# Kernel tuning notes

Measured on AMD Instinct MI355X. Metric: run time of the kernel, lower is better.

The kernel has to match this reference:

```python
import jax, jax.numpy as jnp
import numpy as np

B, CIN, COUT, K = 16, 64, 64, 3
H = W = 192
DEG, HID = 64, 256


def setup_inputs() -> dict:
    key = jax.random.key(0)
    ks = jax.random.split(key, 6)
    x = jax.random.normal(ks[0], (B, CIN, H, W), dtype=jnp.float32)
    degradation_features = jax.random.normal(ks[1], (B, DEG), dtype=jnp.float32)
    # weight_generator: Linear(DEG,256) -> ReLU -> Linear(256, CIN*COUT*K*K)
    W1 = jax.random.normal(ks[2], (DEG, HID), dtype=jnp.float32) * (1.0 / np.sqrt(DEG))
    b1 = jax.random.normal(ks[3], (HID,), dtype=jnp.float32) * 0.01
    W2 = jax.random.normal(ks[4], (HID, CIN * COUT * K * K), dtype=jnp.float32) * (1.0 / np.sqrt(HID))
    b2 = jax.random.normal(ks[5], (CIN * COUT * K * K,), dtype=jnp.float32) * 0.01
    return {"x": x, "degradation_features": degradation_features,
            "W1": W1, "b1": b1, "W2": W2, "b2": b2}


def _forward(x, degradation_features, W1, b1, W2, b2):
    # generate per-sample conv weights: [B, COUT, CIN, K, K] (OIHW)
    h = jax.nn.relu(degradation_features @ W1 + b1)
    weights = (h @ W2 + b2).reshape(B, COUT, CIN, K, K)

    # Per-sample conv2d, NO padding (original loop omits padding arg -> VALID).
    def conv_one(xi, wi):
        # xi: [CIN, H, W], wi: [COUT, CIN, K, K]
        out = jax.lax.conv_general_dilated(
            xi[None], wi, window_strides=(1, 1), padding='VALID',
            dimension_numbers=('NCHW', 'OIHW', 'NCHW'))
        return out[0]  # [COUT, H-K+1, W-K+1]

    return jax.vmap(conv_one)(x, weights)


def reference(x, degradation_features, W1, b1, W2, b2):
    return _forward(x, degradation_features, W1, b1, W2, b2)
```

## Files before the change

kernel.cpp:

```cpp
#include <hip/hip_runtime.h>


typedef __bf16 bf16x8 __attribute__((ext_vector_type(8)));
typedef float  f32x4  __attribute__((ext_vector_type(4)));

#define NB   16
#define CIN  64
#define COUT 64
#define HW   192
#define OHW  190
#define NPIX (HW*HW)
#define NW2  (COUT*CIN*9)

__device__ __forceinline__ unsigned short f2bf(float f) {
    union { float f; unsigned int u; } v; v.f = f;
    unsigned int r = v.u + 0x7FFFu + ((v.u >> 16) & 1u);
    return (unsigned short)(r >> 16);
}
__device__ __forceinline__ float bf2f(unsigned short s) {
    union { unsigned int u; float f; } v; v.u = ((unsigned int)s) << 16;
    return v.f;
}

__device__ __forceinline__ void async_copy16(const void* gsrc, void* ldst) {
    __builtin_amdgcn_global_load_lds(
        (const __attribute__((address_space(1))) unsigned int*)gsrc,
        (__attribute__((address_space(3))) unsigned int*)ldst, 16, 0, 0);
}

__global__ void k1_hidden(const float* __restrict__ deg, const float* __restrict__ W1,
                          const float* __restrict__ b1, float* __restrict__ h) {
    int b = blockIdx.x, j = threadIdx.x;
    float acc = b1[j];
    for (int d = 0; d < 64; ++d) acc += deg[b*64 + d] * W1[d*256 + j];
    h[b*256 + j] = fmaxf(acc, 0.f);
}

__global__ void k2_wgen(const float* __restrict__ h, const float* __restrict__ W2,
                        const float* __restrict__ b2, unsigned short* __restrict__ Aw) {
    __shared__ float hs[16*256];
    __shared__ float red[4][16][65];
    int t = threadIdx.x;
    for (int i = t; i < 16*256; i += 256) hs[i] = h[i];
    __syncthreads();

    int nl = t & 63;
    int kc = t >> 6;
    int n  = blockIdx.x * 64 + nl;
    float acc[16] = {};
    #pragma unroll
    for (int kk = 0; kk < 64; ++kk) {
        int k = kc*64 + kk;
        float w = W2[(size_t)k*NW2 + n];
        #pragma unroll
        for (int b = 0; b < 16; ++b) acc[b] += hs[b*256 + k] * w;
    }
    #pragma unroll
    for (int b = 0; b < 16; ++b) red[kc][b][nl] = acc[b];
    __syncthreads();

    for (int i = t; i < 16*64; i += 256) {
        int b  = i >> 6;
        int nn = i & 63;
        int n2 = blockIdx.x * 64 + nn;
        float s = red[0][b][nn] + red[1][b][nn] + red[2][b][nn] + red[3][b][nn] + b2[n2];
        int co  = n2 / 576;
        int rem = n2 - co*576;
        int ci  = rem / 9;
        int tap = rem - ci*9;
        Aw[(((b*9 + tap)*COUT + co)*CIN) + ci] = f2bf(s);
    }
}

__global__ void k3_transpose(const float* __restrict__ x, unsigned short* __restrict__ xT) {
    __shared__ float tile[64][65];
    int b  = blockIdx.y;
    int p0 = blockIdx.x * 64;
    int t  = threadIdx.x;
    const float* xb = x + (size_t)b * CIN * NPIX;
    {
        int c  = (t & 15) * 4;
        int r0 = t >> 4;
        #pragma unroll
        for (int i = 0; i < 4; ++i) {
            int ci = r0 + 16*i;
            float4 v = *(const float4*)(xb + (size_t)ci*NPIX + p0 + c);
            tile[ci][c] = v.x; tile[ci][c+1] = v.y; tile[ci][c+2] = v.z; tile[ci][c+3] = v.w;
        }
    }
    __syncthreads();
    {
        int ci4 = (t & 15) * 4;
        int pr  = t >> 4;
        #pragma unroll
        for (int i = 0; i < 4; ++i) {
            int pl = pr + 16*i;
            uint2 w;
            w.x = (unsigned int)f2bf(tile[ci4  ][pl]) | ((unsigned int)f2bf(tile[ci4+1][pl]) << 16);
            w.y = (unsigned int)f2bf(tile[ci4+2][pl]) | ((unsigned int)f2bf(tile[ci4+3][pl]) << 16);
            *(uint2*)(&xT[((size_t)b*NPIX + p0 + pl)*CIN + ci4]) = w;
        }
    }
}

#define XS_SLOTS 2816
__global__ __launch_bounds__(256, 3)
void k4_conv(const unsigned short* __restrict__ xT, const unsigned short* __restrict__ Aw,
             float* __restrict__ out) {
    __shared__ unsigned short xs[XS_SLOTS*8];
    const int tid = threadIdx.x;

    int bid = blockIdx.x;
    int wg  = (bid & 7) * 288 + (bid >> 3);
    int b   = wg / 144;
    int ry  = wg - b*144;
    int ty  = ry / 6;
    int tx  = ry - ty*6;
    const int x0 = tx * 32;
    const int y0 = ty * 8;

    const int wv  = tid >> 6;
    const int l   = tid & 63;
    const int l15 = l & 15;
    const int lg  = l >> 4;

    const unsigned short* xTb = xT + (size_t)b * NPIX * CIN;
    #pragma unroll
    for (int it = 0; it < 11; ++it) {
        int s   = it*256 + tid;
        int t   = s >> 3;
        int swc = s & 7;
        int gyl = t / 34;
        int gxl = t - gyl*34;
        int gy  = y0 + gyl; gy = gy > 191 ? 191 : gy;
        int gx  = x0 + gxl; gx = gx > 191 ? 191 : gx;
        const void* src = xTb + ((size_t)(gy*HW + gx))*CIN + ((swc ^ (gx & 7)) * 8);
        void* dst = &xs[(it*256 + wv*64) * 8];
        async_copy16(src, dst);
    }

    const unsigned short* Ab = Aw + b * (9*COUT*CIN);
    const unsigned short* Al = Ab + l15*CIN + lg*8;
    bf16x8 a[2][8];
    #pragma unroll
    for (int cc = 0; cc < 2; ++cc)
        #pragma unroll
        for (int m = 0; m < 4; ++m)
            a[0][cc*4+m] = *(const bf16x8*)(Al + m*1024 + cc*32);

    __syncthreads();

    f32x4 acc[4][4] = {};

    #pragma unroll
    for (int tap = 0; tap < 9; ++tap) {
        const int cur = tap & 1, nxt = cur ^ 1;
        if (tap < 8) {
            #pragma unroll
            for (int cc = 0; cc < 2; ++cc)
                #pragma unroll
                for (int m = 0; m < 4; ++m)
                    a[nxt][cc*4+m] = *(const bf16x8*)(Al + (tap+1)*4096 + m*1024 + cc*32);
        }
        const int ky = tap / 3, kx = tap - 3*(tap/3);
        #pragma unroll
        for (int cc = 0; cc < 2; ++cc) {
            bf16x8 bb[4];
            #pragma unroll
            for (int r = 0; r < 2; ++r)
                #pragma unroll
                for (int xb = 0; xb < 2; ++xb) {
                    int gyl = 2*wv + r + ky;
                    int gxl = xb*16 + l15 + kx;
                    int pch = (cc*4 + lg) ^ (gxl & 7);
                    bb[r*2 + xb] = *(const bf16x8*)(&xs[((gyl*34 + gxl)*8 + pch)*8]);
                }
            #pragma unroll
            for (int m = 0; m < 4; ++m)
                #pragma unroll
                for (int n = 0; n < 4; ++n)
                    acc[m][n] = __builtin_amdgcn_mfma_f32_16x16x32_bf16(a[cur][cc*4+m], bb[n], acc[m][n], 0, 0, 0);
        }
    }

    #pragma unroll
    for (int m = 0; m < 4; ++m)
        #pragma unroll
        for (int r = 0; r < 2; ++r)
            #pragma unroll
            for (int xb = 0; xb < 2; ++xb) {
                int oy = y0 + 2*wv + r;
                int ox = x0 + xb*16 + l15;
                if (oy < OHW && ox < OHW) {
                    f32x4 v = acc[m][r*2 + xb];
                    #pragma unroll
                    for (int j = 0; j < 4; ++j) {
                        int co = m*16 + lg*4 + j;
                        out[(((size_t)(b*COUT + co)*OHW + oy)*OHW) + ox] = v[j];
                    }
                }
            }
}

__global__ void k4_naive(const float* __restrict__ x, const unsigned short* __restrict__ Aw,
                         float* __restrict__ out) {
    int p = blockIdx.x * 256 + threadIdx.x;
    if (p >= OHW*OHW) return;
    int b = blockIdx.z, co = blockIdx.y;
    int oy = p / OHW, ox = p - oy*OHW;
    const float* xb = x + (size_t)b * CIN * NPIX;
    float acc = 0.f;
    for (int ci = 0; ci < CIN; ++ci)
        for (int ky = 0; ky < 3; ++ky) {
            const float* row = xb + ci*NPIX + (oy + ky)*HW + ox;
            #pragma unroll
            for (int kx = 0; kx < 3; ++kx) {
                float w = bf2f(Aw[(((b*9 + ky*3 + kx)*COUT + co)*CIN) + ci]);
                acc += row[kx] * w;
            }
        }
    out[(((b*COUT + co)*OHW + oy)*OHW) + ox] = acc;
}

extern "C" void kernel_launch(void* const* d_in, const int* in_sizes, int n_in,
                              void* d_out, int out_size, void* d_ws, size_t ws_size,
                              hipStream_t stream) {
    const float* x   = (const float*)d_in[0];
    const float* deg = (const float*)d_in[1];
    const float* W1  = (const float*)d_in[2];
    const float* b1  = (const float*)d_in[3];
    const float* W2  = (const float*)d_in[4];
    const float* b2  = (const float*)d_in[5];
    float* out = (float*)d_out;

    const size_t off_h  = 0;
    const size_t off_Aw = 16 * 1024;
    const size_t off_xT = off_Aw + (size_t)NB*9*COUT*CIN*2;
    const size_t need   = off_xT + (size_t)NB*NPIX*CIN*2;

    float* h           = (float*)((char*)d_ws + off_h);
    unsigned short* Aw = (unsigned short*)((char*)d_ws + off_Aw);

    k1_hidden<<<16, 256, 0, stream>>>(deg, W1, b1, h);
    k2_wgen<<<NW2/64, 256, 0, stream>>>(h, W2, b2, Aw);

    if (ws_size >= need) {
        unsigned short* xT = (unsigned short*)((char*)d_ws + off_xT);
        k3_transpose<<<dim3(NPIX/64, NB), 256, 0, stream>>>(x, xT);
        k4_conv<<<2304, 256, 0, stream>>>(xT, Aw, out);
    } else {
        k4_naive<<<dim3((OHW*OHW + 255)/256, COUT, NB), 256, 0, stream>>>(x, Aw, out);
    }
}
```

Measured before the change: 180.4 us.

## Fuse hidden, weight-gen and transpose kernels into one launch; raise MFMA priority

Merges the hidden-layer MLP, weight-generation GEMM and input transpose into a single kernel whose blocks branch by block index. Each weight-gen block recomputes the small hidden layer locally, and the transpose now writes 16-byte packed stores. The aim is to drop two launches and let the weight generation overlap with the transpose. It also adds s_setprio around the MFMA burst in the conv kernel and removes the naive fallback path. The fallback removal assumes the workspace is always large enough, and each weight-gen block now redoes the hidden-layer work.

```diff
diff --git a/kernel.cpp b/kernel.cpp
--- a/kernel.cpp
+++ b/kernel.cpp
@@ -17,10 +17,6 @@
     unsigned int r = v.u + 0x7FFFu + ((v.u >> 16) & 1u);
     return (unsigned short)(r >> 16);
 }
-__device__ __forceinline__ float bf2f(unsigned short s) {
-    union { unsigned int u; float f; } v; v.u = ((unsigned int)s) << 16;
-    return v.f;
-}
 
 __device__ __forceinline__ void async_copy16(const void* gsrc, void* ldst) {
     __builtin_amdgcn_global_load_lds(
@@ -28,77 +24,93 @@
         (__attribute__((address_space(3))) unsigned int*)ldst, 16, 0, 0);
 }
 
-__global__ void k1_hidden(const float* __restrict__ deg, const float* __restrict__ W1,
-                          const float* __restrict__ b1, float* __restrict__ h) {
-    int b = blockIdx.x, j = threadIdx.x;
-    float acc = b1[j];
-    for (int d = 0; d < 64; ++d) acc += deg[b*64 + d] * W1[d*256 + j];
-    h[b*256 + j] = fmaxf(acc, 0.f);
-}
-
-__global__ void k2_wgen(const float* __restrict__ h, const float* __restrict__ W2,
-                        const float* __restrict__ b2, unsigned short* __restrict__ Aw) {
-    __shared__ float hs[16*256];
-    __shared__ float red[4][16][65];
-    int t = threadIdx.x;
-    for (int i = t; i < 16*256; i += 256) hs[i] = h[i];
-    __syncthreads();
-
-    int nl = t & 63;
-    int kc = t >> 6;
-    int n  = blockIdx.x * 64 + nl;
-    float acc[16] = {};
-    #pragma unroll
-    for (int kk = 0; kk < 64; ++kk) {
-        int k = kc*64 + kk;
-        float w = W2[(size_t)k*NW2 + n];
-        #pragma unroll
-        for (int b = 0; b < 16; ++b) acc[b] += hs[b*256 + k] * w;
-    }
-    #pragma unroll
-    for (int b = 0; b < 16; ++b) red[kc][b][nl] = acc[b];
-    __syncthreads();
-
-    for (int i = t; i < 16*64; i += 256) {
-        int b  = i >> 6;
-        int nn = i & 63;
-        int n2 = blockIdx.x * 64 + nn;
-        float s = red[0][b][nn] + red[1][b][nn] + red[2][b][nn] + red[3][b][nn] + b2[n2];
-        int co  = n2 / 576;
-        int rem = n2 - co*576;
-        int ci  = rem / 9;
-        int tap = rem - ci*9;
-        Aw[(((b*9 + tap)*COUT + co)*CIN) + ci] = f2bf(s);
-    }
-}
-
-__global__ void k3_transpose(const float* __restrict__ x, unsigned short* __restrict__ xT) {
-    __shared__ float tile[64][65];
-    int b  = blockIdx.y;
-    int p0 = blockIdx.x * 64;
-    int t  = threadIdx.x;
-    const float* xb = x + (size_t)b * CIN * NPIX;
-    {
-        int c  = (t & 15) * 4;
-        int r0 = t >> 4;
-        #pragma unroll
-        for (int i = 0; i < 4; ++i) {
-            int ci = r0 + 16*i;
-            float4 v = *(const float4*)(xb + (size_t)ci*NPIX + p0 + c);
-            tile[ci][c] = v.x; tile[ci][c+1] = v.y; tile[ci][c+2] = v.z; tile[ci][c+3] = v.w;
-        }
-    }
-    __syncthreads();
-    {
-        int ci4 = (t & 15) * 4;
-        int pr  = t >> 4;
-        #pragma unroll
-        for (int i = 0; i < 4; ++i) {
-            int pl = pr + 16*i;
-            uint2 w;
-            w.x = (unsigned int)f2bf(tile[ci4  ][pl]) | ((unsigned int)f2bf(tile[ci4+1][pl]) << 16);
-            w.y = (unsigned int)f2bf(tile[ci4+2][pl]) | ((unsigned int)f2bf(tile[ci4+3][pl]) << 16);
-            *(uint2*)(&xT[((size_t)b*NPIX + p0 + pl)*CIN + ci4]) = w;
+__global__ __launch_bounds__(256)
+void k23(const float* __restrict__ x, unsigned short* __restrict__ xT,
+         const float* __restrict__ deg, const float* __restrict__ W1,
+         const float* __restrict__ b1, const float* __restrict__ W2,
+         const float* __restrict__ b2, unsigned short* __restrict__ Aw) {
+    __shared__ __align__(16) char smem[37376];
+    const int bid = blockIdx.x;
+    const int t   = threadIdx.x;
+
+    if (bid < 9216) {
+        float (*tile)[65] = (float (*)[65])smem;
+        int b  = bid / 576;
+        int p0 = (bid - b*576) * 64;
+        const float* xb = x + (size_t)b * CIN * NPIX;
+        {
+            int c  = (t & 15) * 4;
+            int r0 = t >> 4;
+            #pragma unroll
+            for (int i = 0; i < 4; ++i) {
+                int ci = r0 + 16*i;
+                float4 v = *(const float4*)(xb + (size_t)ci*NPIX + p0 + c);
+                tile[ci][c] = v.x; tile[ci][c+1] = v.y; tile[ci][c+2] = v.z; tile[ci][c+3] = v.w;
+            }
+        }
+        __syncthreads();
+        {
+            int ci8 = (t & 7) * 8;
+            int pr0 = t >> 3;
+            #pragma unroll
+            for (int i = 0; i < 2; ++i) {
+                int pl = pr0 + 32*i;
+                union { uint4 v; unsigned short u[8]; } pk;
+                #pragma unroll
+                for (int j = 0; j < 8; ++j) pk.u[j] = f2bf(tile[ci8 + j][pl]);
+                *(uint4*)(&xT[((size_t)b*NPIX + p0 + pl)*CIN + ci8]) = pk.v;
+            }
+        }
+    } else {
+        float* degs = (float*)smem;
+        float* hs   = degs + 16*64;
+        float (*red)[16][33] = (float (*)[16][33])(hs + 16*256);
+        int nb = bid - 9216;
+
+        for (int i = t; i < 16*64; i += 256) degs[i] = deg[i];
+        __syncthreads();
+        {
+            float acc[16];
+            float bias = b1[t];
+            #pragma unroll
+            for (int bb2 = 0; bb2 < 16; ++bb2) acc[bb2] = bias;
+            for (int d = 0; d < 64; ++d) {
+                float w = W1[d*256 + t];
+                #pragma unroll
+                for (int bb2 = 0; bb2 < 16; ++bb2) acc[bb2] += degs[bb2*64 + d] * w;
+            }
+            #pragma unroll
+            for (int bb2 = 0; bb2 < 16; ++bb2) hs[bb2*256 + t] = fmaxf(acc[bb2], 0.f);
+        }
+        __syncthreads();
+
+        int nl = t & 31;
+        int kc = t >> 5;
+        int n  = nb * 32 + nl;
+        float acc[16] = {};
+        #pragma unroll
+        for (int kk = 0; kk < 32; ++kk) {
+            int k = kc*32 + kk;
+            float w = W2[(size_t)k*NW2 + n];
+            #pragma unroll
+            for (int b = 0; b < 16; ++b) acc[b] += hs[b*256 + k] * w;
+        }
+        #pragma unroll
+        for (int b = 0; b < 16; ++b) red[kc][b][nl] = acc[b];
+        __syncthreads();
+
+        for (int i = t; i < 512; i += 256) {
+            int b  = i >> 5;
+            int nn = i & 31;
+            int n2 = nb * 32 + nn;
+            float s = b2[n2];
+            #pragma unroll
+            for (int k = 0; k < 8; ++k) s += red[k][b][nn];
+            int co  = n2 / 576;
+            int rem = n2 - co*576;
+            int ci  = rem / 9;
+            int tap = rem - ci*9;
+            Aw[(((b*9 + tap)*COUT + co)*CIN) + ci] = f2bf(s);
         }
     }
 }
@@ -175,11 +187,13 @@
                     int pch = (cc*4 + lg) ^ (gxl & 7);
                     bb[r*2 + xb] = *(const bf16x8*)(&xs[((gyl*34 + gxl)*8 + pch)*8]);
                 }
+            __builtin_amdgcn_s_setprio(1);
             #pragma unroll
             for (int m = 0; m < 4; ++m)
                 #pragma unroll
                 for (int n = 0; n < 4; ++n)
                     acc[m][n] = __builtin_amdgcn_mfma_f32_16x16x32_bf16(a[cur][cc*4+m], bb[n], acc[m][n], 0, 0, 0);
+            __builtin_amdgcn_s_setprio(0);
         }
     }
 
@@ -196,30 +210,10 @@
                     #pragma unroll
                     for (int j = 0; j < 4; ++j) {
                         int co = m*16 + lg*4 + j;
-                        out[(((size_t)(b*COUT + co)*OHW + oy)*OHW) + ox] = v[j];
+                        out[((size_t)(b*COUT + co)*OHW + oy)*OHW + ox] = v[j];
                     }
                 }
             }
-}
-
-__global__ void k4_naive(const float* __restrict__ x, const unsigned short* __restrict__ Aw,
-                         float* __restrict__ out) {
-    int p = blockIdx.x * 256 + threadIdx.x;
-    if (p >= OHW*OHW) return;
-    int b = blockIdx.z, co = blockIdx.y;
-    int oy = p / OHW, ox = p - oy*OHW;
-    const float* xb = x + (size_t)b * CIN * NPIX;
-    float acc = 0.f;
-    for (int ci = 0; ci < CIN; ++ci)
-        for (int ky = 0; ky < 3; ++ky) {
-            const float* row = xb + ci*NPIX + (oy + ky)*HW + ox;
-            #pragma unroll
-            for (int kx = 0; kx < 3; ++kx) {
-                float w = bf2f(Aw[(((b*9 + ky*3 + kx)*COUT + co)*CIN) + ci]);
-                acc += row[kx] * w;
-            }
-        }
-    out[(((b*COUT + co)*OHW + oy)*OHW) + ox] = acc;
 }
 
 extern "C" void kernel_launch(void* const* d_in, const int* in_sizes, int n_in,
@@ -233,22 +227,9 @@
     const float* b2  = (const float*)d_in[5];
     float* out = (float*)d_out;
 
-    const size_t off_h  = 0;
-    const size_t off_Aw = 16 * 1024;
-    const size_t off_xT = off_Aw + (size_t)NB*9*COUT*CIN*2;
-    const size_t need   = off_xT + (size_t)NB*NPIX*CIN*2;
-
-    float* h           = (float*)((char*)d_ws + off_h);
-    unsigned short* Aw = (unsigned short*)((char*)d_ws + off_Aw);
-
-    k1_hidden<<<16, 256, 0, stream>>>(deg, W1, b1, h);
-    k2_wgen<<<NW2/64, 256, 0, stream>>>(h, W2, b2, Aw);
-
-    if (ws_size >= need) {
-        unsigned short* xT = (unsigned short*)((char*)d_ws + off_xT);
-        k3_transpose<<<dim3(NPIX/64, NB), 256, 0, stream>>>(x, xT);
-        k4_conv<<<2304, 256, 0, stream>>>(xT, Aw, out);
-    } else {
-        k4_naive<<<dim3((OHW*OHW + 255)/256, COUT, NB), 256, 0, stream>>>(x, Aw, out);
-    }
-}
+    unsigned short* Aw = (unsigned short*)d_ws;
+    unsigned short* xT = (unsigned short*)((char*)d_ws + (size_t)NB*9*COUT*CIN*2);
+
+    k23<<<9216 + 1152, 256, 0, stream>>>(x, xT, deg, W1, b1, W2, b2, Aw);
+    k4_conv<<<2304, 256, 0, stream>>>(xT, Aw, out);
+}
```

New measurement: 189.2 us. 4.9% more time.
